# Kernel optimization log

Hardware: AMD Instinct MI355X
Metric: run time of the kernel (lower is better)

The kernel has to match this reference:

```python
import jax, jax.numpy as jnp
import numpy as np

LAYER_BS = 63
N_SITES = 12
B = 2048


def _kaiming_uniform(key, shape, fan_in):
    # torch kaiming_uniform_ with a=0: bound = sqrt(6/fan_in)
    bound = np.sqrt(6.0 / fan_in)
    return jax.random.uniform(key, shape, jnp.float32, -bound, bound)


def _cnn12(x, w):
    # x: (B, L, 12, Cin); w: (L, 3*Cin, Cout)
    nn0 = jnp.roll(x, -1, axis=-2) + jnp.roll(x, 3, axis=-2)
    nnn0 = jnp.roll(x, -2, axis=-2) + jnp.roll(x, 4, axis=-2)
    c0 = jnp.concatenate([nn0, nnn0], axis=-1)          # (B,L,12,2*Cin)
    c1 = c0 + jnp.roll(c0, -2, axis=-2)
    allc = jnp.concatenate([x, c1], axis=-1)            # (B,L,12,3*Cin)
    return jnp.einsum('blsc,lco->blso', allc, w)


def _batch_linear(x, w, b):
    # x: (B, L, F); w: (L, F, O); b: (L, O)
    return jnp.einsum('blf,lfo->blo', x, w) + b


def setup_inputs() -> dict:
    key = jax.random.key(0)
    ks = jax.random.split(key, 9)
    zs = jax.random.normal(ks[0], (B, LAYER_BS, N_SITES, 2), jnp.float32)
    # CNN weights: (L, 3*Cin, Cout); kaiming fan_in = 3*Cin
    w1 = _kaiming_uniform(ks[1], (LAYER_BS, 6, 32), 6)
    w2 = _kaiming_uniform(ks[2], (LAYER_BS, 96, 64), 96)
    fw1 = _kaiming_uniform(ks[3], (LAYER_BS, 128, 64), 128)
    fb1 = jax.random.uniform(ks[4], (LAYER_BS, 64), jnp.float32, -1 / np.sqrt(128), 1 / np.sqrt(128))
    fw2 = _kaiming_uniform(ks[5], (LAYER_BS, 64, 64), 64)
    fb2 = jax.random.uniform(ks[6], (LAYER_BS, 64), jnp.float32, -1 / np.sqrt(64), 1 / np.sqrt(64))
    fw3 = _kaiming_uniform(ks[7], (LAYER_BS, 64, 1), 64)
    fb3 = jax.random.uniform(ks[8], (LAYER_BS, 1), jnp.float32, -1 / np.sqrt(64), 1 / np.sqrt(64))
    return {"zs": zs, "w1": w1, "w2": w2, "fw1": fw1, "fb1": fb1,
            "fw2": fw2, "fb2": fb2, "fw3": fw3, "fb3": fb3}


def reference(zs, w1, w2, fw1, fb1, fw2, fb2, fw3, fb3):
    h = jax.nn.relu(_cnn12(zs, w1))                     # (B,L,12,32)
    h = jax.nn.relu(_cnn12(h, w2))                      # (B,L,12,64)
    h = jnp.concatenate([h.mean(axis=-2), h.max(axis=-2)], axis=-1)
    h = jax.nn.relu(_batch_linear(h, fw1, fb1))
    h = jax.nn.relu(_batch_linear(h, fw2, fb2))
    out = _batch_linear(h, fw3, fb3)                    # (B,L,1)
    return out[..., 0]                                  # (B,L)
```

## Files before the change

kernel.cpp:

```cpp
#include <hip/hip_runtime.h>


#define LNUM 63
#define BT 16
#define NBT 128
#define WSL 19968

typedef __attribute__((ext_vector_type(8))) _Float16 half8;
typedef __attribute__((ext_vector_type(2))) _Float16 half2v;
typedef __attribute__((ext_vector_type(4))) float floatx4;
typedef __attribute__((ext_vector_type(4))) unsigned uint4v;

static __device__ __forceinline__ unsigned cvtpk(float a, float b) {
    return __builtin_bit_cast(unsigned, __builtin_amdgcn_cvt_pkrtz(a, b));
}
static __device__ __forceinline__ half2v u2h(unsigned u) { return __builtin_bit_cast(half2v, u); }
static __device__ __forceinline__ unsigned h2u(half2v h) { return __builtin_bit_cast(unsigned, h); }
static __device__ __forceinline__ half2v hmax2(half2v a, half2v b) {
    half2v r;
    r[0] = a[0] > b[0] ? a[0] : b[0];
    r[1] = a[1] > b[1] ? a[1] : b[1];
    return r;
}
static __device__ __forceinline__ float hlo16(unsigned short s) {
    return (float)__builtin_bit_cast(_Float16, s);
}
static __device__ __forceinline__ int w12(int v) { return v >= 12 ? v - 12 : v; }
static __device__ __forceinline__ float2 add2(float2 a, float2 b) { return make_float2(a.x + b.x, a.y + b.y); }

#define H2S    130
#define O_POOL 16640
#define O_POOL2 0
#define O_G2   1280

__global__ void prep(const float* __restrict__ w2, const float* __restrict__ fw1,
                     const float* __restrict__ fw2, unsigned short* __restrict__ ws) {
    const int l = blockIdx.x, t = threadIdx.x;
    const int o = t & 63, g = t >> 6;
    if (blockIdx.y == 0) {
        unsigned* w2t = (unsigned*)(ws + (size_t)l * WSL);
        const float* w2l = w2 + (size_t)l * 6144;
        #pragma unroll
        for (int i = 0; i < 12; ++i) {
            int cp = g + 4 * i, c = 2 * cp;
            w2t[o * 52 + cp] = cvtpk(w2l[c * 64 + o], w2l[(c + 1) * 64 + o]);
        }
    } else {
        unsigned* f1t = (unsigned*)(ws + (size_t)l * WSL + 6656);
        const float* f1l = fw1 + (size_t)l * 8192;
        #pragma unroll
        for (int i = 0; i < 16; ++i) {
            int cp = g + 4 * i;
            f1t[o * 68 + cp] = cvtpk(f1l[cp * 64 + o], f1l[(64 + cp) * 64 + o]);
        }
        unsigned* f2t = (unsigned*)(ws + (size_t)l * WSL + 15360);
        const float* f2l = fw2 + (size_t)l * 4096;
        #pragma unroll
        for (int i = 0; i < 8; ++i) {
            int cp = g + 4 * i, c = 2 * cp;
            f2t[o * 36 + cp] = cvtpk(f2l[c * 64 + o], f2l[(c + 1) * 64 + o]);
        }
    }
}

__global__ __launch_bounds__(256, 4) void fused_nn(
    const float* __restrict__ zs,  const float* __restrict__ w1,
    const float* __restrict__ fb1, const float* __restrict__ fb2,
    const float* __restrict__ fw3, const float* __restrict__ fb3,
    const unsigned short* __restrict__ ws,
    float* __restrict__ out)
{
    __shared__ __align__(16) unsigned short U[18816];

    const int t    = threadIdx.x;
    const int lane = t & 63;
    const int wv   = t >> 6;
    const int n    = lane & 15;
    const int quad = lane >> 4;
    const int l    = blockIdx.x / NBT;
    const int b0   = (blockIdx.x % NBT) * BT;

    {
        const int b = t >> 4, cpair = t & 15, c0 = cpair * 2;
        const float* xb = zs + ((size_t)(b0 + b) * LNUM + l) * 24;
        float4 xq[6];
        #pragma unroll
        for (int q = 0; q < 6; ++q) xq[q] = *(const float4*)(xb + q * 4);
        float2 xv[12], xr[12], xA[12], xB[12];
        #pragma unroll
        for (int s = 0; s < 12; ++s)
            xv[s] = (s & 1) ? make_float2(xq[s >> 1].z, xq[s >> 1].w)
                            : make_float2(xq[s >> 1].x, xq[s >> 1].y);
        #pragma unroll
        for (int s = 0; s < 12; ++s) xr[s] = add2(xv[w12(s + 1)], xv[w12(s + 11)]);
        #pragma unroll
        for (int s = 0; s < 12; ++s) {
            xA[s] = add2(xr[w12(s + 2)], xr[w12(s + 10)]);
            xB[s] = add2(xr[w12(s + 3)], xr[w12(s + 9)]);
        }
        const float* wl = w1 + (size_t)l * 192 + c0;
        const float2 w0  = *(const float2*)(wl);
        const float2 w1v = *(const float2*)(wl + 32);
        const float2 w2v = *(const float2*)(wl + 64);
        const float2 w3v = *(const float2*)(wl + 96);
        const float2 w4v = *(const float2*)(wl + 128);
        const float2 w5v = *(const float2*)(wl + 160);
        unsigned hp[12];
        #pragma unroll
        for (int s = 0; s < 12; ++s) {
            float hx = xv[s].x*w0.x + xv[s].y*w1v.x + xA[s].x*w2v.x + xA[s].y*w3v.x
                     + xB[s].x*w4v.x + xB[s].y*w5v.x;
            float hy = xv[s].x*w0.y + xv[s].y*w1v.y + xA[s].x*w2v.y + xA[s].y*w3v.y
                     + xB[s].x*w4v.y + xB[s].y*w5v.y;
            hp[s] = cvtpk(fmaxf(hx, 0.f), fmaxf(hy, 0.f));
        }
        half2v hh[12], hr[12];
        #pragma unroll
        for (int s = 0; s < 12; ++s) hh[s] = u2h(hp[s]);
        #pragma unroll
        for (int s = 0; s < 12; ++s) hr[s] = hh[w12(s + 1)] + hh[w12(s + 11)];
        unsigned* dwU = (unsigned*)U;
        const int g = cpair >> 2, jj = cpair & 3;
        #pragma unroll
        for (int s = 0; s < 12; ++s) {
            half2v hA = hr[w12(s + 2)] + hr[w12(s + 10)];
            half2v hB = hr[w12(s + 3)] + hr[w12(s + 9)];
            const int row = b * 12 + s;
            const int base = row * 48 + ((g ^ (s & 3)) << 2) + jj;
            dwU[base]      = hp[s];
            dwU[base + 16] = h2u(hA);
            dwU[base + 32] = h2u(hB);
        }
    }
    __syncthreads();

    floatx4 acc[3][4];
    #pragma unroll
    for (int mi = 0; mi < 3; ++mi)
        #pragma unroll
        for (int nt = 0; nt < 4; ++nt) acc[mi][nt] = (floatx4){0.f, 0.f, 0.f, 0.f};
    {
        half8 af[3][3];
        const int sw = (quad ^ (n & 3)) * 8;
        #pragma unroll
        for (int mi = 0; mi < 3; ++mi) {
            const int row = (3 * wv + mi) * 16 + n;
            #pragma unroll
            for (int ks = 0; ks < 3; ++ks)
                af[mi][ks] = *(const half8*)(U + row * 96 + ks * 32 + sw);
        }
        const uint4v* w2q = (const uint4v*)(ws + (size_t)l * WSL);
        #pragma unroll
        for (int ks = 0; ks < 3; ++ks) {
            uint4v bw[4];
            #pragma unroll
            for (int nt = 0; nt < 4; ++nt)
                bw[nt] = w2q[(nt * 16 + n) * 13 + ks * 4 + quad];
            #pragma unroll
            for (int mi = 0; mi < 3; ++mi)
                #pragma unroll
                for (int nt = 0; nt < 4; ++nt)
                    acc[mi][nt] = __builtin_amdgcn_mfma_f32_16x16x32_f16(
                        af[mi][ks], __builtin_bit_cast(half8, bw[nt]), acc[mi][nt], 0, 0, 0);
        }
    }
    __syncthreads();

    #pragma unroll
    for (int mi = 0; mi < 3; ++mi) {
        const int r0g  = (3 * wv + mi) * 16 + quad * 4;
        const int bidx = r0g / 12;
        const int s0   = r0g - bidx * 12;
        const int dbase = bidx * 8 + (s0 >> 1);
        #pragma unroll
        for (int nt = 0; nt < 4; ++nt) {
            const int o = nt * 16 + n;
            uint2 v;
            v.x = cvtpk(fmaxf(acc[mi][nt][0], 0.f), fmaxf(acc[mi][nt][1], 0.f));
            v.y = cvtpk(fmaxf(acc[mi][nt][2], 0.f), fmaxf(acc[mi][nt][3], 0.f));
            *(uint2*)((unsigned*)U + o * H2S + dbase) = v;
        }
    }
    __syncthreads();

    {
        const int o = lane;
        #pragma unroll
        for (int bb = 0; bb < 4; ++bb) {
            const int b = wv * 4 + bb;
            const unsigned* src = (const unsigned*)U + o * H2S + b * 8;
            uint2 p0 = *(const uint2*)(src);
            uint2 p1 = *(const uint2*)(src + 2);
            uint2 p2 = *(const uint2*)(src + 4);
            half2v v0 = u2h(p0.x), v1 = u2h(p0.y), v2 = u2h(p1.x);
            half2v v3 = u2h(p1.y), v4 = u2h(p2.x), v5 = u2h(p2.y);
            half2v sm = ((v0 + v1) + (v2 + v3)) + (v4 + v5);
            half2v mx = hmax2(hmax2(hmax2(v0, v1), hmax2(v2, v3)), hmax2(v4, v5));
            float s = (float)sm[0] + (float)sm[1];
            float m = fmaxf((float)mx[0], (float)mx[1]);
            ((unsigned*)U)[O_POOL / 2 + b * 68 + o] = cvtpk(s * (1.f / 12.f), m);
        }
    }
    __syncthreads();

    {
        const int o = wv * 16 + n;
        const float bias = fb1[(size_t)l * 64 + o];
        floatx4 a1 = (floatx4){bias, bias, bias, bias};
        const uint4v* f1q = (const uint4v*)(ws + (size_t)l * WSL + 6656);
        #pragma unroll
        for (int ks = 0; ks < 4; ++ks) {
            half8 av = *(const half8*)(U + O_POOL + n * 136 + ks * 32 + quad * 8);
            uint4v bw = f1q[o * 17 + ks * 4 + quad];
            a1 = __builtin_amdgcn_mfma_f32_16x16x32_f16(av, __builtin_bit_cast(half8, bw), a1, 0, 0, 0);
        }
        __syncthreads();
        #pragma unroll
        for (int i = 0; i < 2; ++i) {
            unsigned pk = cvtpk(fmaxf(a1[2 * i], 0.f), fmaxf(a1[2 * i + 1], 0.f));
            U[O_POOL2 + (quad * 4 + 2 * i)     * 72 + o] = (unsigned short)(pk & 0xffffu);
            U[O_POOL2 + (quad * 4 + 2 * i + 1) * 72 + o] = (unsigned short)(pk >> 16);
        }
    }
    __syncthreads();

    {
        const int o = wv * 16 + n;
        const float bias = fb2[(size_t)l * 64 + o];
        floatx4 a2 = (floatx4){bias, bias, bias, bias};
        const uint4v* f2q = (const uint4v*)(ws + (size_t)l * WSL + 15360);
        #pragma unroll
        for (int ks = 0; ks < 2; ++ks) {
            half8 av = *(const half8*)(U + O_POOL2 + n * 72 + ks * 32 + quad * 8);
            uint4v bw = f2q[o * 9 + ks * 4 + quad];
            a2 = __builtin_amdgcn_mfma_f32_16x16x32_f16(av, __builtin_bit_cast(half8, bw), a2, 0, 0, 0);
        }
        #pragma unroll
        for (int i = 0; i < 2; ++i) {
            unsigned pk = cvtpk(fmaxf(a2[2 * i], 0.f), fmaxf(a2[2 * i + 1], 0.f));
            U[O_G2 + (quad * 4 + 2 * i)     * 72 + o] = (unsigned short)(pk & 0xffffu);
            U[O_G2 + (quad * 4 + 2 * i + 1) * 72 + o] = (unsigned short)(pk >> 16);
        }
    }
    __syncthreads();

    if (t < 16) {
        float a = fb3[l];
        const float* w3 = fw3 + (size_t)l * 64;
        #pragma unroll
        for (int c4 = 0; c4 < 16; ++c4) {
            uint2 u2 = *(const uint2*)(U + O_G2 + t * 72 + c4 * 4);
            float4 w = *(const float4*)(w3 + c4 * 4);
            a += hlo16((unsigned short)(u2.x & 0xffff)) * w.x
               + hlo16((unsigned short)(u2.x >> 16))    * w.y
               + hlo16((unsigned short)(u2.y & 0xffff)) * w.z
               + hlo16((unsigned short)(u2.y >> 16))    * w.w;
        }
        out[(size_t)(b0 + t) * LNUM + l] = a;
    }
}

extern "C" void kernel_launch(void* const* d_in, const int* in_sizes, int n_in,
                              void* d_out, int out_size, void* d_ws, size_t ws_size,
                              hipStream_t stream) {
    const float* zs  = (const float*)d_in[0];
    const float* w1  = (const float*)d_in[1];
    const float* w2  = (const float*)d_in[2];
    const float* fw1 = (const float*)d_in[3];
    const float* fb1 = (const float*)d_in[4];
    const float* fw2 = (const float*)d_in[5];
    const float* fb2 = (const float*)d_in[6];
    const float* fw3 = (const float*)d_in[7];
    const float* fb3 = (const float*)d_in[8];
    float* out = (float*)d_out;
    unsigned short* ws = (unsigned short*)d_ws;

    hipLaunchKernelGGL(prep, dim3(LNUM, 2), dim3(256), 0, stream, w2, fw1, fw2, ws);
    hipLaunchKernelGGL(fused_nn, dim3(LNUM * NBT), dim3(256), 0, stream,
                       zs, w1, fb1, fb2, fw3, fb3, ws, out);
}
```

Baseline: 137.3 us.

## Shrink shared memory by building conv2 neighbor sums on the fly and fusing pooling

Layer-1 output is now stored once per site in a compact 20-dword-stride layout. The neighbor-sum operands for the second convolution are rebuilt from four LDS loads plus half adds just before each MFMA, instead of being precomputed and stored three times. Pooling partials (sum and max over 4 sites) are reduced in registers from the MFMA accumulators, and the final pool step reads only three partials per channel. Shared memory falls from about 37KB to about 16.6KB and the launch bounds target 6 blocks per CU, trading extra LDS reads and f16 adds in the conv2 loop for higher occupancy.

```diff
diff --git a/kernel.cpp b/kernel.cpp
--- a/kernel.cpp
+++ b/kernel.cpp
@@ -16,22 +16,16 @@
 }
 static __device__ __forceinline__ half2v u2h(unsigned u) { return __builtin_bit_cast(half2v, u); }
 static __device__ __forceinline__ unsigned h2u(half2v h) { return __builtin_bit_cast(unsigned, h); }
-static __device__ __forceinline__ half2v hmax2(half2v a, half2v b) {
-    half2v r;
-    r[0] = a[0] > b[0] ? a[0] : b[0];
-    r[1] = a[1] > b[1] ? a[1] : b[1];
-    return r;
-}
 static __device__ __forceinline__ float hlo16(unsigned short s) {
     return (float)__builtin_bit_cast(_Float16, s);
 }
 static __device__ __forceinline__ int w12(int v) { return v >= 12 ? v - 12 : v; }
 static __device__ __forceinline__ float2 add2(float2 a, float2 b) { return make_float2(a.x + b.x, a.y + b.y); }
 
-#define H2S    130
-#define O_POOL 16640
-#define O_POOL2 0
-#define O_G2   1280
+#define O_POOLDW 3072
+#define O_POOLUS 6144
+#define O_POOL2  0
+#define O_G2     1280
 
 __global__ void prep(const float* __restrict__ w2, const float* __restrict__ fw1,
                      const float* __restrict__ fw2, unsigned short* __restrict__ ws) {
@@ -63,14 +57,15 @@
     }
 }
 
-__global__ __launch_bounds__(256, 4) void fused_nn(
+__global__ __launch_bounds__(256, 6) void fused_nn(
     const float* __restrict__ zs,  const float* __restrict__ w1,
     const float* __restrict__ fb1, const float* __restrict__ fb2,
     const float* __restrict__ fw3, const float* __restrict__ fb3,
     const unsigned short* __restrict__ ws,
     float* __restrict__ out)
 {
-    __shared__ __align__(16) unsigned short U[18816];
+    __shared__ __align__(16) unsigned U[4160];
+    unsigned short* USH = (unsigned short*)U;
 
     const int t    = threadIdx.x;
     const int lane = t & 63;
@@ -105,31 +100,13 @@
         const float2 w3v = *(const float2*)(wl + 96);
         const float2 w4v = *(const float2*)(wl + 128);
         const float2 w5v = *(const float2*)(wl + 160);
-        unsigned hp[12];
         #pragma unroll
         for (int s = 0; s < 12; ++s) {
             float hx = xv[s].x*w0.x + xv[s].y*w1v.x + xA[s].x*w2v.x + xA[s].y*w3v.x
                      + xB[s].x*w4v.x + xB[s].y*w5v.x;
             float hy = xv[s].x*w0.y + xv[s].y*w1v.y + xA[s].x*w2v.y + xA[s].y*w3v.y
                      + xB[s].x*w4v.y + xB[s].y*w5v.y;
-            hp[s] = cvtpk(fmaxf(hx, 0.f), fmaxf(hy, 0.f));
-        }
-        half2v hh[12], hr[12];
-        #pragma unroll
-        for (int s = 0; s < 12; ++s) hh[s] = u2h(hp[s]);
-        #pragma unroll
-        for (int s = 0; s < 12; ++s) hr[s] = hh[w12(s + 1)] + hh[w12(s + 11)];
-        unsigned* dwU = (unsigned*)U;
-        const int g = cpair >> 2, jj = cpair & 3;
-        #pragma unroll
-        for (int s = 0; s < 12; ++s) {
-            half2v hA = hr[w12(s + 2)] + hr[w12(s + 10)];
-            half2v hB = hr[w12(s + 3)] + hr[w12(s + 9)];
-            const int row = b * 12 + s;
-            const int base = row * 48 + ((g ^ (s & 3)) << 2) + jj;
-            dwU[base]      = hp[s];
-            dwU[base + 16] = h2u(hA);
-            dwU[base + 32] = h2u(hB);
+            U[(b * 12 + s) * 20 + cpair] = cvtpk(fmaxf(hx, 0.f), fmaxf(hy, 0.f));
         }
     }
     __syncthreads();
@@ -140,66 +117,89 @@
         #pragma unroll
         for (int nt = 0; nt < 4; ++nt) acc[mi][nt] = (floatx4){0.f, 0.f, 0.f, 0.f};
     {
-        half8 af[3][3];
-        const int sw = (quad ^ (n & 3)) * 8;
+        int bi[3], si[3];
         #pragma unroll
         for (int mi = 0; mi < 3; ++mi) {
-            const int row = (3 * wv + mi) * 16 + n;
-            #pragma unroll
-            for (int ks = 0; ks < 3; ++ks)
-                af[mi][ks] = *(const half8*)(U + row * 96 + ks * 32 + sw);
-        }
+            int row = 48 * wv + 16 * mi + n;
+            bi[mi] = row / 12;
+            si[mi] = row - 12 * bi[mi];
+        }
+        const int q4 = quad * 4;
         const uint4v* w2q = (const uint4v*)(ws + (size_t)l * WSL);
+        const int dA[4] = {1, 11, 3, 9};
+        const int dB[4] = {2, 10, 4, 8};
         #pragma unroll
         for (int ks = 0; ks < 3; ++ks) {
             uint4v bw[4];
             #pragma unroll
             for (int nt = 0; nt < 4; ++nt)
                 bw[nt] = w2q[(nt * 16 + n) * 13 + ks * 4 + quad];
+            half8 af[3];
+            #pragma unroll
+            for (int mi = 0; mi < 3; ++mi) {
+                const int rb = bi[mi] * 12, s = si[mi];
+                if (ks == 0) {
+                    af[mi] = *(const half8*)(U + (rb + s) * 20 + q4);
+                } else {
+                    const int* d = (ks == 1) ? dA : dB;
+                    half8 l0 = *(const half8*)(U + (rb + w12(s + d[0])) * 20 + q4);
+                    half8 l1 = *(const half8*)(U + (rb + w12(s + d[1])) * 20 + q4);
+                    half8 l2 = *(const half8*)(U + (rb + w12(s + d[2])) * 20 + q4);
+                    half8 l3 = *(const half8*)(U + (rb + w12(s + d[3])) * 20 + q4);
+                    af[mi] = (l0 + l1) + (l2 + l3);
+                }
+            }
             #pragma unroll
             for (int mi = 0; mi < 3; ++mi)
                 #pragma unroll
                 for (int nt = 0; nt < 4; ++nt)
                     acc[mi][nt] = __builtin_amdgcn_mfma_f32_16x16x32_f16(
-                        af[mi][ks], __builtin_bit_cast(half8, bw[nt]), acc[mi][nt], 0, 0, 0);
+                        af[mi], __builtin_bit_cast(half8, bw[nt]), acc[mi][nt], 0, 0, 0);
         }
     }
     __syncthreads();
 
     #pragma unroll
     for (int mi = 0; mi < 3; ++mi) {
-        const int r0g  = (3 * wv + mi) * 16 + quad * 4;
-        const int bidx = r0g / 12;
-        const int s0   = r0g - bidx * 12;
-        const int dbase = bidx * 8 + (s0 >> 1);
+        const int rr = 48 * wv + 16 * mi + 4 * quad;
+        const int bq = rr / 12;
+        const int chk = (rr - 12 * bq) >> 2;
         #pragma unroll
         for (int nt = 0; nt < 4; ++nt) {
-            const int o = nt * 16 + n;
-            uint2 v;
-            v.x = cvtpk(fmaxf(acc[mi][nt][0], 0.f), fmaxf(acc[mi][nt][1], 0.f));
-            v.y = cvtpk(fmaxf(acc[mi][nt][2], 0.f), fmaxf(acc[mi][nt][3], 0.f));
-            *(uint2*)((unsigned*)U + o * H2S + dbase) = v;
-        }
-    }
-    __syncthreads();
-
-    {
-        const int o = lane;
-        #pragma unroll
-        for (int bb = 0; bb < 4; ++bb) {
-            const int b = wv * 4 + bb;
-            const unsigned* src = (const unsigned*)U + o * H2S + b * 8;
-            uint2 p0 = *(const uint2*)(src);
-            uint2 p1 = *(const uint2*)(src + 2);
-            uint2 p2 = *(const uint2*)(src + 4);
-            half2v v0 = u2h(p0.x), v1 = u2h(p0.y), v2 = u2h(p1.x);
-            half2v v3 = u2h(p1.y), v4 = u2h(p2.x), v5 = u2h(p2.y);
-            half2v sm = ((v0 + v1) + (v2 + v3)) + (v4 + v5);
-            half2v mx = hmax2(hmax2(hmax2(v0, v1), hmax2(v2, v3)), hmax2(v4, v5));
-            float s = (float)sm[0] + (float)sm[1];
-            float m = fmaxf((float)mx[0], (float)mx[1]);
-            ((unsigned*)U)[O_POOL / 2 + b * 68 + o] = cvtpk(s * (1.f / 12.f), m);
-        }
+            const int ch = nt * 16 + n;
+            float r0 = fmaxf(acc[mi][nt][0], 0.f), r1 = fmaxf(acc[mi][nt][1], 0.f);
+            float r2 = fmaxf(acc[mi][nt][2], 0.f), r3 = fmaxf(acc[mi][nt][3], 0.f);
+            float sm = (r0 + r1) + (r2 + r3);
+            float mx = fmaxf(fmaxf(r0, r1), fmaxf(r2, r3));
+            U[(bq * 64 + ch) * 3 + chk] = cvtpk(sm, mx);
+        }
+    }
+    __syncthreads();
+
+    {
+        const unsigned* p = U + t * 12;
+        uint4v q0 = *(const uint4v*)(p);
+        uint4v q1 = *(const uint4v*)(p + 4);
+        uint4v q2 = *(const uint4v*)(p + 8);
+        unsigned arr[12] = {q0.x, q0.y, q0.z, q0.w, q1.x, q1.y, q1.z, q1.w,
+                            q2.x, q2.y, q2.z, q2.w};
+        const int b = t >> 4, ch0 = (t * 4) & 63;
+        const _Float16 inv12 = (_Float16)(1.0f / 12.0f);
+        unsigned pk[4];
+        #pragma unroll
+        for (int j = 0; j < 4; ++j) {
+            half2v d0 = u2h(arr[3 * j]), d1 = u2h(arr[3 * j + 1]), d2 = u2h(arr[3 * j + 2]);
+            _Float16 s = (d0[0] + d1[0]) + d2[0];
+            _Float16 m0 = d0[1] > d1[1] ? d0[1] : d1[1];
+            _Float16 m  = m0 > d2[1] ? m0 : d2[1];
+            half2v pm;
+            pm[0] = s * inv12;
+            pm[1] = m;
+            pk[j] = h2u(pm);
+        }
+        uint2 w01 = make_uint2(pk[0], pk[1]), w23 = make_uint2(pk[2], pk[3]);
+        *(uint2*)(U + O_POOLDW + b * 68 + ch0)     = w01;
+        *(uint2*)(U + O_POOLDW + b * 68 + ch0 + 2) = w23;
     }
     __syncthreads();
 
@@ -210,16 +210,15 @@
         const uint4v* f1q = (const uint4v*)(ws + (size_t)l * WSL + 6656);
         #pragma unroll
         for (int ks = 0; ks < 4; ++ks) {
-            half8 av = *(const half8*)(U + O_POOL + n * 136 + ks * 32 + quad * 8);
+            half8 av = *(const half8*)(USH + O_POOLUS + n * 136 + ks * 32 + quad * 8);
             uint4v bw = f1q[o * 17 + ks * 4 + quad];
             a1 = __builtin_amdgcn_mfma_f32_16x16x32_f16(av, __builtin_bit_cast(half8, bw), a1, 0, 0, 0);
         }
-        __syncthreads();
         #pragma unroll
         for (int i = 0; i < 2; ++i) {
             unsigned pk = cvtpk(fmaxf(a1[2 * i], 0.f), fmaxf(a1[2 * i + 1], 0.f));
-            U[O_POOL2 + (quad * 4 + 2 * i)     * 72 + o] = (unsigned short)(pk & 0xffffu);
-            U[O_POOL2 + (quad * 4 + 2 * i + 1) * 72 + o] = (unsigned short)(pk >> 16);
+            USH[O_POOL2 + (quad * 4 + 2 * i)     * 72 + o] = (unsigned short)(pk & 0xffffu);
+            USH[O_POOL2 + (quad * 4 + 2 * i + 1) * 72 + o] = (unsigned short)(pk >> 16);
         }
     }
     __syncthreads();
@@ -231,15 +230,15 @@
         const uint4v* f2q = (const uint4v*)(ws + (size_t)l * WSL + 15360);
         #pragma unroll
         for (int ks = 0; ks < 2; ++ks) {
-            half8 av = *(const half8*)(U + O_POOL2 + n * 72 + ks * 32 + quad * 8);
+            half8 av = *(const half8*)(USH + O_POOL2 + n * 72 + ks * 32 + quad * 8);
             uint4v bw = f2q[o * 9 + ks * 4 + quad];
             a2 = __builtin_amdgcn_mfma_f32_16x16x32_f16(av, __builtin_bit_cast(half8, bw), a2, 0, 0, 0);
         }
         #pragma unroll
         for (int i = 0; i < 2; ++i) {
             unsigned pk = cvtpk(fmaxf(a2[2 * i], 0.f), fmaxf(a2[2 * i + 1], 0.f));
-            U[O_G2 + (quad * 4 + 2 * i)     * 72 + o] = (unsigned short)(pk & 0xffffu);
-            U[O_G2 + (quad * 4 + 2 * i + 1) * 72 + o] = (unsigned short)(pk >> 16);
+            USH[O_G2 + (quad * 4 + 2 * i)     * 72 + o] = (unsigned short)(pk & 0xffffu);
+            USH[O_G2 + (quad * 4 + 2 * i + 1) * 72 + o] = (unsigned short)(pk >> 16);
         }
     }
     __syncthreads();
@@ -249,7 +248,7 @@
         const float* w3 = fw3 + (size_t)l * 64;
         #pragma unroll
         for (int c4 = 0; c4 < 16; ++c4) {
-            uint2 u2 = *(const uint2*)(U + O_G2 + t * 72 + c4 * 4);
+            uint2 u2 = *(const uint2*)(USH + O_G2 + t * 72 + c4 * 4);
             float4 w = *(const float4*)(w3 + c4 * 4);
             a += hlo16((unsigned short)(u2.x & 0xffff)) * w.x
                + hlo16((unsigned short)(u2.x >> 16))    * w.y
```

Result: slower. 291.2 us (+112.1%).
